# Kernel tuning notes

Measured on AMD Instinct MI355X. Metric: run time of the kernel, lower is better.

The kernel has to match this reference:

```python
import jax, jax.numpy as jnp
import numpy as np

N_EMB = 1024
N_HEAD = 16
HEAD_DIM = N_EMB // N_HEAD


def setup_inputs() -> dict:
    key = jax.random.key(0)
    ks = jax.random.split(key, 5)
    scale = 0.02
    x = jax.random.normal(ks[0], (2, 2048, N_EMB), dtype=jnp.float32)
    W_attn = jax.random.normal(ks[1], (N_EMB, 3 * N_EMB), dtype=jnp.float32) * scale
    b_attn = jnp.zeros((3 * N_EMB,), dtype=jnp.float32)
    W_proj = jax.random.normal(ks[2], (N_EMB, N_EMB), dtype=jnp.float32) * scale
    b_proj = jnp.zeros((N_EMB,), dtype=jnp.float32)
    return {"x": x, "W_attn": W_attn, "b_attn": b_attn, "W_proj": W_proj, "b_proj": b_proj}


def reference(x, W_attn, b_attn, W_proj, b_proj):
    B, T, C = x.shape
    qkv = x @ W_attn + b_attn  # [B, T, 3C]
    q, k, v = jnp.split(qkv, 3, axis=-1)
    # [B, H, T, Dh]
    q = q.reshape(B, T, N_HEAD, HEAD_DIM).transpose(0, 2, 1, 3)
    k = k.reshape(B, T, N_HEAD, HEAD_DIM).transpose(0, 2, 1, 3)
    v = v.reshape(B, T, N_HEAD, HEAD_DIM).transpose(0, 2, 1, 3)
    scale = 1.0 / jnp.sqrt(jnp.float32(HEAD_DIM))
    attn = jnp.einsum('bhqd,bhkd->bhqk', q, k) * scale  # [B, H, T, T]
    causal = jnp.tril(jnp.ones((T, T), dtype=bool))
    attn = jnp.where(causal[None, None], attn, -jnp.inf)
    attn = jax.nn.softmax(attn, axis=-1)
    y = jnp.einsum('bhqk,bhkd->bhqd', attn, v)  # [B, H, T, Dh]
    y = y.transpose(0, 2, 1, 3).reshape(B, T, C)
    return y @ W_proj + b_proj
```

## Files before the change

kernel.cpp:

```cpp
#include <hip/hip_runtime.h>
#include <hip/hip_bf16.h>

typedef __bf16 bf16;
typedef __attribute__((ext_vector_type(2))) __bf16 bf16x2;
typedef __attribute__((ext_vector_type(4))) __bf16 bf16x4;
typedef __attribute__((ext_vector_type(8))) __bf16 bf16x8;
typedef __attribute__((ext_vector_type(4))) float f32x4;
typedef __attribute__((ext_vector_type(16))) float f32x16;
typedef unsigned int u32;
typedef __attribute__((ext_vector_type(4))) u32 u32x4;
typedef const __attribute__((address_space(1))) u32* gptr_t;
typedef __attribute__((address_space(3))) u32* lptr_t;

#define N_EMB 1024
#define N_HEAD 16
#define HEAD_DIM 64
#define T_SEQ 2048
#define BATCH 2
#define M_TOT (BATCH * T_SEQ)
#define N_QKV (3 * N_EMB)
#define KDIM 1024
#define CS_LOG2E 0.1803368801111129f

__device__ inline unsigned short f2bu(float f) {
    unsigned u = __builtin_bit_cast(unsigned, f);
    return (unsigned short)((u + 0x7fffu + ((u >> 16) & 1u)) >> 16);
}
__device__ inline bf16 f2b(float f) {
    unsigned short s = f2bu(f);
    return __builtin_bit_cast(bf16, s);
}
__device__ inline u32 pkbf(float lo, float hi) {
    bf16x2 t; t[0] = (bf16)lo; t[1] = (bf16)hi;
    return __builtin_bit_cast(u32, t);
}
__device__ __forceinline__ float xhalf_max(float x) {
    return fmaxf(x, __shfl_xor(x, 32, 64));
}
__device__ __forceinline__ float xhalf_sum(float x) {
    return x + __shfl_xor(x, 32, 64);
}

__global__ __launch_bounds__(256) void k_cast(const float* __restrict__ x,
                                              bf16* __restrict__ xb, int n4) {
    int i = blockIdx.x * 256 + threadIdx.x;
    if (i < n4) {
        float4 v = reinterpret_cast<const float4*>(x)[i];
        ushort4 u;
        u.x = f2bu(v.x); u.y = f2bu(v.y); u.z = f2bu(v.z); u.w = f2bu(v.w);
        reinterpret_cast<ushort4*>(xb)[i] = u;
    }
}

__global__ __launch_bounds__(256) void k_transpose(const float* __restrict__ W,
                                                   bf16* __restrict__ Wt,
                                                   int K, int N) {
    __shared__ float tile[32][33];
    int k0 = blockIdx.x * 32;
    int n0 = blockIdx.y * 32;
    int tx = threadIdx.x & 31;
    int ty = threadIdx.x >> 5;
    for (int j = 0; j < 32; j += 8)
        tile[ty + j][tx] = W[(k0 + ty + j) * N + n0 + tx];
    __syncthreads();
    for (int j = 0; j < 32; j += 8)
        Wt[(n0 + ty + j) * (long)K + k0 + tx] = f2b(tile[tx][ty + j]);
}

__global__ __launch_bounds__(256) void k_vtrans(const bf16* __restrict__ v,
                                                bf16* __restrict__ vt) {
    __shared__ bf16 tile[64 * 76];
    const int bh = blockIdx.y;
    const int t0 = blockIdx.x * 64;
    const bf16* src = v + (size_t)bh * T_SEQ * HEAD_DIM;
    bf16* dst = vt + (size_t)bh * HEAD_DIM * T_SEQ;
    const int tid = threadIdx.x;
    #pragma unroll
    for (int it = 0; it < 2; ++it) {
        const int row = (tid >> 3) + it * 32;
        const int col = (tid & 7) * 8;
        bf16x8 val = *reinterpret_cast<const bf16x8*>(src + (size_t)(t0 + row) * HEAD_DIM + col);
        bf16x4 lo;  lo[0] = val[0]; lo[1] = val[1]; lo[2] = val[2]; lo[3] = val[3];
        bf16x4 hiv; hiv[0] = val[4]; hiv[1] = val[5]; hiv[2] = val[6]; hiv[3] = val[7];
        *reinterpret_cast<bf16x4*>(&tile[row * 76 + col]) = lo;
        *reinterpret_cast<bf16x4*>(&tile[row * 76 + col + 4]) = hiv;
    }
    __syncthreads();
    #pragma unroll
    for (int it = 0; it < 2; ++it) {
        const int d  = (tid >> 3) + it * 32;
        const int tt = (tid & 7) * 8;
        bf16x8 val;
        #pragma unroll
        for (int q = 0; q < 8; ++q)
            val[q] = tile[(tt + q) * 76 + d];
        *reinterpret_cast<bf16x8*>(dst + (size_t)d * T_SEQ + t0 + tt) = val;
    }
}

#define GEMM_MAINLOOP(A_, Bt_, m0_, n0_)                                          \
    __shared__ __align__(16) bf16 As[128 * 32];                                   \
    __shared__ __align__(16) bf16 Bs[128 * 32];                                   \
    const int lane = threadIdx.x & 63;                                            \
    const int w    = threadIdx.x >> 6;                                            \
    const int wr   = w >> 1;                                                      \
    const int wc   = w & 1;                                                       \
    const int r    = lane & 15;                                                   \
    const int ko   = (lane >> 4) * 8;                                             \
    const int srow = w * 32 + (lane >> 2);                                        \
    const int sk   = (lane & 3) * 8;                                              \
    const bf16* a_g0 = A_ + (size_t)(m0_ + srow) * KDIM + sk;                     \
    const bf16* a_g1 = a_g0 + 16 * KDIM;                                          \
    const bf16* b_g0 = Bt_ + (size_t)(n0_ + srow) * KDIM + sk;                    \
    const bf16* b_g1 = b_g0 + 16 * KDIM;                                          \
    bf16* a_l0 = As + (w * 2) * 512;                                              \
    bf16* a_l1 = As + (w * 2 + 1) * 512;                                          \
    bf16* b_l0 = Bs + (w * 2) * 512;                                              \
    bf16* b_l1 = Bs + (w * 2 + 1) * 512;                                          \
    f32x4 acc[4][4];                                                              \
    for (int i = 0; i < 4; ++i)                                                   \
        for (int j = 0; j < 4; ++j) acc[i][j] = (f32x4){0.f, 0.f, 0.f, 0.f};      \
    for (int k0 = 0; k0 < KDIM; k0 += 32) {                                       \
        __builtin_amdgcn_global_load_lds((gptr_t)(const void*)(a_g0 + k0),        \
                                         (lptr_t)(void*)a_l0, 16, 0, 0);          \
        __builtin_amdgcn_global_load_lds((gptr_t)(const void*)(a_g1 + k0),        \
                                         (lptr_t)(void*)a_l1, 16, 0, 0);          \
        __builtin_amdgcn_global_load_lds((gptr_t)(const void*)(b_g0 + k0),        \
                                         (lptr_t)(void*)b_l0, 16, 0, 0);          \
        __builtin_amdgcn_global_load_lds((gptr_t)(const void*)(b_g1 + k0),        \
                                         (lptr_t)(void*)b_l1, 16, 0, 0);          \
        __syncthreads();                                                          \
        bf16x8 af[4], bfr[4];                                                     \
        for (int m = 0; m < 4; ++m)                                               \
            af[m] = *reinterpret_cast<const bf16x8*>(As + (wr * 64 + m * 16 + r) * 32 + ko); \
        for (int n = 0; n < 4; ++n)                                               \
            bfr[n] = *reinterpret_cast<const bf16x8*>(Bs + (wc * 64 + n * 16 + r) * 32 + ko); \
        for (int m = 0; m < 4; ++m)                                               \
            for (int n = 0; n < 4; ++n)                                           \
                acc[m][n] = __builtin_amdgcn_mfma_f32_16x16x32_bf16(af[m], bfr[n], acc[m][n], 0, 0, 0); \
        __syncthreads();                                                          \
    }

#define GEMM_MAINLOOP_64(A_, Bt_, m0_, n0_)                                       \
    __shared__ __align__(16) bf16 As[64 * 32];                                    \
    __shared__ __align__(16) bf16 Bs[128 * 32];                                   \
    const int lane = threadIdx.x & 63;                                            \
    const int w    = threadIdx.x >> 6;                                            \
    const int wr   = w >> 1;                                                      \
    const int wc   = w & 1;                                                       \
    const int r    = lane & 15;                                                   \
    const int ko   = (lane >> 4) * 8;                                             \
    const int srow = w * 16 + (lane >> 2);                                        \
    const int sk   = (lane & 3) * 8;                                              \
    const bf16* a_g0 = A_ + (size_t)(m0_ + srow) * KDIM + sk;                     \
    const bf16* b_g0 = Bt_ + (size_t)(n0_ + srow) * KDIM + sk;                    \
    const bf16* b_g1 = b_g0 + 64 * KDIM;                                          \
    bf16* a_l0 = As + w * 512;                                                    \
    bf16* b_l0 = Bs + w * 512;                                                    \
    bf16* b_l1 = Bs + 64 * 32 + w * 512;                                          \
    f32x4 acc[2][4];                                                              \
    for (int i = 0; i < 2; ++i)                                                   \
        for (int j = 0; j < 4; ++j) acc[i][j] = (f32x4){0.f, 0.f, 0.f, 0.f};      \
    for (int k0 = 0; k0 < KDIM; k0 += 32) {                                       \
        __builtin_amdgcn_global_load_lds((gptr_t)(const void*)(a_g0 + k0),        \
                                         (lptr_t)(void*)a_l0, 16, 0, 0);          \
        __builtin_amdgcn_global_load_lds((gptr_t)(const void*)(b_g0 + k0),        \
                                         (lptr_t)(void*)b_l0, 16, 0, 0);          \
        __builtin_amdgcn_global_load_lds((gptr_t)(const void*)(b_g1 + k0),        \
                                         (lptr_t)(void*)b_l1, 16, 0, 0);          \
        __syncthreads();                                                          \
        bf16x8 af[2], bfr[4];                                                     \
        for (int m = 0; m < 2; ++m)                                               \
            af[m] = *reinterpret_cast<const bf16x8*>(As + (wr * 32 + m * 16 + r) * 32 + ko); \
        for (int n = 0; n < 4; ++n)                                               \
            bfr[n] = *reinterpret_cast<const bf16x8*>(Bs + (wc * 64 + n * 16 + r) * 32 + ko); \
        for (int m = 0; m < 2; ++m)                                               \
            for (int n = 0; n < 4; ++n)                                           \
                acc[m][n] = __builtin_amdgcn_mfma_f32_16x16x32_bf16(af[m], bfr[n], acc[m][n], 0, 0, 0); \
        __syncthreads();                                                          \
    }

__global__ __launch_bounds__(256) void k_gemm_qkv(const bf16* __restrict__ A,
                                                  const bf16* __restrict__ Bt,
                                                  const float* __restrict__ bias,
                                                  bf16* __restrict__ qb,
                                                  bf16* __restrict__ kb,
                                                  bf16* __restrict__ vb) {
    const int m0 = blockIdx.x * 128;
    const int n0 = blockIdx.y * 128;
    GEMM_MAINLOOP(A, Bt, m0, n0)
    const int col   = lane & 15;
    const int rbase = (lane >> 4) * 4;
    for (int nn = 0; nn < 4; ++nn) {
        int n = n0 + wc * 64 + nn * 16 + col;
        float bv = bias[n];
        int which = n >> 10;
        int c  = n & 1023;
        int h  = c >> 6;
        int dh = c & 63;
        bf16* dst = (which == 0) ? qb : ((which == 1) ? kb : vb);
        const float sc = (which == 0) ? CS_LOG2E : 1.0f;
        for (int mm = 0; mm < 4; ++mm) {
            for (int i = 0; i < 4; ++i) {
                int m = m0 + wr * 64 + mm * 16 + rbase + i;
                int b_ = m >> 11;
                int t  = m & 2047;
                dst[(((b_ * N_HEAD + h) * T_SEQ) + t) * HEAD_DIM + dh] =
                    f2b((acc[mm][nn][i] + bv) * sc);
            }
        }
    }
}

__global__ __launch_bounds__(256) void k_gemm_proj(const bf16* __restrict__ A,
                                                   const bf16* __restrict__ Bt,
                                                   const float* __restrict__ bias,
                                                   float* __restrict__ out) {
    const int m0 = blockIdx.x * 64;
    const int n0 = blockIdx.y * 128;
    GEMM_MAINLOOP_64(A, Bt, m0, n0)
    const int col   = lane & 15;
    const int rbase = (lane >> 4) * 4;
    for (int nn = 0; nn < 4; ++nn) {
        int n = n0 + wc * 64 + nn * 16 + col;
        float bv = bias[n];
        for (int mm = 0; mm < 2; ++mm) {
            for (int i = 0; i < 4; ++i) {
                int m = m0 + wr * 32 + mm * 16 + rbase + i;
                out[(size_t)m * N_EMB + n] = acc[mm][nn][i] + bv;
            }
        }
    }
}

__device__ __forceinline__ void pv_group(const float* p, int hi,
                                         const bf16x8 (&va)[2][2], f32x16 (&o)[2]) {
    u32 c[8], sw[8];
    #pragma unroll
    for (int i = 0; i < 8; ++i) c[i] = pkbf(p[2 * i], p[2 * i + 1]);
    #pragma unroll
    for (int i = 0; i < 8; ++i) sw[i] = __shfl_xor(c[i], 32, 64);
    u32x4 f0, f1;
    f0[0] = hi ? sw[2] : c[0];  f0[1] = hi ? sw[3] : c[1];
    f0[2] = hi ? c[2]  : sw[0]; f0[3] = hi ? c[3]  : sw[1];
    f1[0] = hi ? sw[6] : c[4];  f1[1] = hi ? sw[7] : c[5];
    f1[2] = hi ? c[6]  : sw[4]; f1[3] = hi ? c[7]  : sw[5];
    bf16x8 pb0 = __builtin_bit_cast(bf16x8, f0);
    bf16x8 pb1 = __builtin_bit_cast(bf16x8, f1);
    __builtin_amdgcn_s_setprio(1);
    #pragma unroll
    for (int dt = 0; dt < 2; ++dt) {
        o[dt] = __builtin_amdgcn_mfma_f32_32x32x16_bf16(va[dt][0], pb0, o[dt], 0, 0, 0);
        o[dt] = __builtin_amdgcn_mfma_f32_32x32x16_bf16(va[dt][1], pb1, o[dt], 0, 0, 0);
    }
    __builtin_amdgcn_s_setprio(0);
}

__device__ __forceinline__ void load_va(const bf16* __restrict__ Vt, int kbase,
                                        int qr, int hi, bf16x8 (&va)[2][2]) {
    #pragma unroll
    for (int dt = 0; dt < 2; ++dt)
        #pragma unroll
        for (int ks = 0; ks < 2; ++ks)
            va[dt][ks] = *reinterpret_cast<const bf16x8*>(
                Vt + (size_t)(dt * 32 + qr) * T_SEQ + kbase + ks * 16 + hi * 8);
}

__device__ __forceinline__ float tree_max16(const f32x16& v) {
    float a0 = fmaxf(v[0], v[1]),   a1 = fmaxf(v[2], v[3]);
    float a2 = fmaxf(v[4], v[5]),   a3 = fmaxf(v[6], v[7]);
    float a4 = fmaxf(v[8], v[9]),   a5 = fmaxf(v[10], v[11]);
    float a6 = fmaxf(v[12], v[13]), a7 = fmaxf(v[14], v[15]);
    float b0 = fmaxf(a0, a1), b1 = fmaxf(a2, a3);
    float b2 = fmaxf(a4, a5), b3 = fmaxf(a6, a7);
    return fmaxf(fmaxf(b0, b1), fmaxf(b2, b3));
}

template<bool DIAG_HI>
__device__ __forceinline__ void attn_tile64(
    const bf16* __restrict__ K, const bf16* __restrict__ Vt, int kbase,
    int qr, int hi, const bf16x8 (&qf)[4],
    float& m_r, float& l_r, f32x16 (&o)[2]) {
    bf16x8 kf0[4], kf1[4];
    #pragma unroll
    for (int f = 0; f < 4; ++f) {
        kf0[f] = *reinterpret_cast<const bf16x8*>(
            K + (size_t)(kbase + qr) * HEAD_DIM + f * 16 + hi * 8);
        kf1[f] = *reinterpret_cast<const bf16x8*>(
            K + (size_t)(kbase + 32 + qr) * HEAD_DIM + f * 16 + hi * 8);
    }
    f32x16 st0, st1;
    #pragma unroll
    for (int r = 0; r < 16; ++r) { st0[r] = 0.f; st1[r] = 0.f; }
    __builtin_amdgcn_s_setprio(1);
    #pragma unroll
    for (int f = 0; f < 4; ++f)
        st0 = __builtin_amdgcn_mfma_f32_32x32x16_bf16(kf0[f], qf[f], st0, 0, 0, 0);
    #pragma unroll
    for (int f = 0; f < 4; ++f)
        st1 = __builtin_amdgcn_mfma_f32_32x32x16_bf16(kf1[f], qf[f], st1, 0, 0, 0);
    __builtin_amdgcn_s_setprio(0);
    if (DIAG_HI) {
        const int kp4 = 4 * hi;
        #pragma unroll
        for (int r = 0; r < 16; ++r) {
            const int kpos = (r & 3) + 8 * (r >> 2) + kp4;
            if (kpos > qr) st1[r] = -3.0e38f;
        }
    }
    float mt = fmaxf(tree_max16(st0), tree_max16(st1));
    mt = xhalf_max(mt);
    if (!__all(mt <= m_r + 8.f)) {
        const float mn = fmaxf(m_r, mt);
        const float alpha = exp2f(m_r - mn);
        m_r = mn;
        l_r *= alpha;
        #pragma unroll
        for (int r = 0; r < 16; ++r) { o[0][r] *= alpha; o[1][r] *= alpha; }
    }
    bf16x8 va0[2][2];
    load_va(Vt, kbase, qr, hi, va0);
    float p0[16], p1[16];
    #pragma unroll
    for (int r = 0; r < 16; ++r) { p0[r] = exp2f(st0[r] - m_r); }
    #pragma unroll
    for (int r = 0; r < 16; ++r) { p1[r] = exp2f(st1[r] - m_r); }
    float s0 = 0.f, s1 = 0.f;
    #pragma unroll
    for (int r = 0; r < 8; ++r) { s0 += p0[r] + p0[r + 8]; s1 += p1[r] + p1[r + 8]; }
    l_r += xhalf_sum(s0 + s1);
    pv_group(p0, hi, va0, o);
    bf16x8 va1[2][2];
    load_va(Vt, kbase + 32, qr, hi, va1);
    pv_group(p1, hi, va1, o);
}

template<bool DIAG_MASK>
__device__ __forceinline__ void attn_tile32(
    const bf16* __restrict__ K, const bf16* __restrict__ Vt, int kbase,
    int qr, int hi, const bf16x8 (&qf)[4],
    float& m_r, float& l_r, f32x16 (&o)[2]) {
    bf16x8 kf[4];
    #pragma unroll
    for (int f = 0; f < 4; ++f)
        kf[f] = *reinterpret_cast<const bf16x8*>(
            K + (size_t)(kbase + qr) * HEAD_DIM + f * 16 + hi * 8);
    f32x16 st;
    #pragma unroll
    for (int r = 0; r < 16; ++r) st[r] = 0.f;
    __builtin_amdgcn_s_setprio(1);
    #pragma unroll
    for (int f = 0; f < 4; ++f)
        st = __builtin_amdgcn_mfma_f32_32x32x16_bf16(kf[f], qf[f], st, 0, 0, 0);
    __builtin_amdgcn_s_setprio(0);
    if (DIAG_MASK) {
        const int kp4 = 4 * hi;
        #pragma unroll
        for (int r = 0; r < 16; ++r) {
            const int kpos = (r & 3) + 8 * (r >> 2) + kp4;
            if (kpos > qr) st[r] = -3.0e38f;
        }
    }
    float mt = xhalf_max(tree_max16(st));
    if (!__all(mt <= m_r + 8.f)) {
        const float mn = fmaxf(m_r, mt);
        const float alpha = exp2f(m_r - mn);
        m_r = mn;
        l_r *= alpha;
        #pragma unroll
        for (int r = 0; r < 16; ++r) { o[0][r] *= alpha; o[1][r] *= alpha; }
    }
    bf16x8 va[2][2];
    load_va(Vt, kbase, qr, hi, va);
    float p[16];
    #pragma unroll
    for (int r = 0; r < 16; ++r) p[r] = exp2f(st[r] - m_r);
    float s = 0.f;
    #pragma unroll
    for (int r = 0; r < 8; ++r) s += p[r] + p[r + 8];
    l_r += xhalf_sum(s);
    pv_group(p, hi, va, o);
}

__global__ __launch_bounds__(128, 3) void k_attn(const bf16* __restrict__ qb,
                                                 const bf16* __restrict__ kb,
                                                 const bf16* __restrict__ vtb,
                                                 bf16* __restrict__ yb) {
    const int lane = threadIdx.x & 63;
    const int wv   = threadIdx.x >> 6;
    const int bh   = blockIdx.x;
    const int qblk = 63 - blockIdx.y;
    const int q0   = qblk * 32;
    const int b    = bh >> 4;
    const int h    = bh & 15;

    const bf16* Q  = qb  + (size_t)bh * T_SEQ * HEAD_DIM;
    const bf16* K  = kb  + (size_t)bh * T_SEQ * HEAD_DIM;
    const bf16* Vt = vtb + (size_t)bh * HEAD_DIM * T_SEQ;

    const int qr = lane & 31;
    const int hi = lane >> 5;

    bf16x8 qf[4];
    #pragma unroll
    for (int f = 0; f < 4; ++f)
        qf[f] = *reinterpret_cast<const bf16x8*>(
            Q + (size_t)(q0 + qr) * HEAD_DIM + f * 16 + hi * 8);

    f32x16 o[2];
    #pragma unroll
    for (int r = 0; r < 16; ++r) { o[0][r] = 0.f; o[1][r] = 0.f; }
    float m_r = -3.0e38f, l_r = 0.f;

    const int n  = qblk + 1;
    const int h0 = n - (n >> 1);
    const int lo  = wv ? h0 : 0;
    const int end = wv ? n  : h0;
    const bool has_diag = (end == n) && (end > lo);
    const int nd_end = has_diag ? end - 1 : end;

    int t = lo;
    while (t + 2 <= nd_end) {
        attn_tile64<false>(K, Vt, t * 32, qr, hi, qf, m_r, l_r, o);
        t += 2;
    }
    if (has_diag) {
        if (nd_end - t == 1)
            attn_tile64<true>(K, Vt, t * 32, qr, hi, qf, m_r, l_r, o);
        else
            attn_tile32<true>(K, Vt, qblk * 32, qr, hi, qf, m_r, l_r, o);
    } else if (t < end) {
        attn_tile32<false>(K, Vt, t * 32, qr, hi, qf, m_r, l_r, o);
    }

    __shared__ float ls_o[64][33];
    __shared__ float ls_m[64];
    __shared__ float ls_l[64];
    if (wv == 1) {
        #pragma unroll
        for (int i = 0; i < 16; ++i) {
            ls_o[lane][i]      = o[0][i];
            ls_o[lane][16 + i] = o[1][i];
        }
        ls_m[lane] = m_r;
        ls_l[lane] = l_r;
    }
    __syncthreads();
    if (wv == 1) return;
    const float m1 = ls_m[lane];
    const float l1 = ls_l[lane];
    const float mN = fmaxf(m_r, m1);
    const float a0 = exp2f(m_r - mN);
    const float a1 = (m1 > -1.0e37f) ? exp2f(m1 - mN) : 0.f;
    l_r = l_r * a0 + l1 * a1;
    #pragma unroll
    for (int i = 0; i < 16; ++i) {
        o[0][i] = o[0][i] * a0 + ls_o[lane][i]      * a1;
        o[1][i] = o[1][i] * a0 + ls_o[lane][16 + i] * a1;
    }

    const float inv = 1.f / fmaxf(l_r, 1e-30f);
    const int tq = q0 + qr;
    bf16* yrow = yb + ((size_t)(b * T_SEQ + tq)) * N_EMB + h * HEAD_DIM;
    #pragma unroll
    for (int dt = 0; dt < 2; ++dt) {
        #pragma unroll
        for (int rr = 0; rr < 4; ++rr) {
            const int d0 = dt * 32 + 8 * rr + 4 * hi;
            ushort4 u;
            u.x = f2bu(o[dt][4 * rr + 0] * inv);
            u.y = f2bu(o[dt][4 * rr + 1] * inv);
            u.z = f2bu(o[dt][4 * rr + 2] * inv);
            u.w = f2bu(o[dt][4 * rr + 3] * inv);
            *reinterpret_cast<ushort4*>(yrow + d0) = u;
        }
    }
}

extern "C" void kernel_launch(void* const* d_in, const int* in_sizes, int n_in,
                              void* d_out, int out_size, void* d_ws, size_t ws_size,
                              hipStream_t stream) {
    const float* x      = (const float*)d_in[0];
    const float* W_attn = (const float*)d_in[1];
    const float* b_attn = (const float*)d_in[2];
    const float* W_proj = (const float*)d_in[3];
    const float* b_proj = (const float*)d_in[4];
    float* out = (float*)d_out;

    const size_t sz_x   = (size_t)M_TOT * N_EMB;
    const size_t sz_wat = (size_t)N_QKV * N_EMB;
    const size_t sz_wpt = (size_t)N_EMB * N_EMB;
    const size_t sz_hd  = (size_t)BATCH * N_HEAD * T_SEQ * HEAD_DIM;
    const size_t need = (sz_x + sz_wat + sz_wpt + 3 * sz_hd + sz_x) * sizeof(bf16);
    if (ws_size < need) return;

    bf16* xb  = (bf16*)d_ws;
    bf16* wat = xb + sz_x;
    bf16* wpt = wat + sz_wat;
    bf16* qb  = wpt + sz_wpt;
    bf16* kbf = qb + sz_hd;
    bf16* vbf = kbf + sz_hd;
    bf16* yb  = vbf + sz_hd;
    bf16* vtb = xb;

    k_cast<<<dim3((sz_x / 4 + 255) / 256), 256, 0, stream>>>(x, xb, (int)(sz_x / 4));
    k_transpose<<<dim3(N_EMB / 32, N_QKV / 32), 256, 0, stream>>>(W_attn, wat, N_EMB, N_QKV);
    k_transpose<<<dim3(N_EMB / 32, N_EMB / 32), 256, 0, stream>>>(W_proj, wpt, N_EMB, N_EMB);
    k_gemm_qkv<<<dim3(M_TOT / 128, N_QKV / 128), 256, 0, stream>>>(xb, wat, b_attn, qb, kbf, vbf);
    k_vtrans<<<dim3(T_SEQ / 64, BATCH * N_HEAD), 256, 0, stream>>>(vbf, vtb);
    k_attn<<<dim3(BATCH * N_HEAD, 64), 128, 0, stream>>>(qb, kbf, vtb, yb);
    k_gemm_proj<<<dim3(M_TOT / 64, N_EMB / 128), 256, 0, stream>>>(yb, wpt, b_proj, out);
}
```

Baseline: 139.2 us.

## Split attention KV range across four waves per query block instead of two

```diff
diff --git a/kernel.cpp b/kernel.cpp
--- a/kernel.cpp
+++ b/kernel.cpp
@@ -382,10 +382,10 @@
     pv_group(p, hi, va, o);
 }
 
-__global__ __launch_bounds__(128, 3) void k_attn(const bf16* __restrict__ qb,
-                                                 const bf16* __restrict__ kb,
-                                                 const bf16* __restrict__ vtb,
-                                                 bf16* __restrict__ yb) {
+__global__ __launch_bounds__(256) void k_attn(const bf16* __restrict__ qb,
+                                              const bf16* __restrict__ kb,
+                                              const bf16* __restrict__ vtb,
+                                              bf16* __restrict__ yb) {
     const int lane = threadIdx.x & 63;
     const int wv   = threadIdx.x >> 6;
     const int bh   = blockIdx.x;
@@ -412,11 +412,13 @@
     for (int r = 0; r < 16; ++r) { o[0][r] = 0.f; o[1][r] = 0.f; }
     float m_r = -3.0e38f, l_r = 0.f;
 
-    const int n  = qblk + 1;
-    const int h0 = n - (n >> 1);
-    const int lo  = wv ? h0 : 0;
-    const int end = wv ? n  : h0;
-    const bool has_diag = (end == n) && (end > lo);
+    const int n    = qblk + 1;
+    const int base = n >> 2;
+    const int rem  = n & 3;
+    const int lo   = wv * base + (wv < rem ? wv : rem);
+    const int cnt  = base + (wv < rem ? 1 : 0);
+    const int end  = lo + cnt;
+    const bool has_diag = (end == n) && (cnt > 0);
     const int nd_end = has_diag ? end - 1 : end;
 
     int t = lo;
@@ -428,35 +430,41 @@
         if (nd_end - t == 1)
             attn_tile64<true>(K, Vt, t * 32, qr, hi, qf, m_r, l_r, o);
         else
-            attn_tile32<true>(K, Vt, qblk * 32, qr, hi, qf, m_r, l_r, o);
+            attn_tile32<true>(K, Vt, (n - 1) * 32, qr, hi, qf, m_r, l_r, o);
     } else if (t < end) {
         attn_tile32<false>(K, Vt, t * 32, qr, hi, qf, m_r, l_r, o);
     }
 
-    __shared__ float ls_o[64][33];
-    __shared__ float ls_m[64];
-    __shared__ float ls_l[64];
-    if (wv == 1) {
+    __shared__ float ls_o[3][64][33];
+    __shared__ float ls_m[3][64];
+    __shared__ float ls_l[3][64];
+    if (wv > 0) {
         #pragma unroll
         for (int i = 0; i < 16; ++i) {
-            ls_o[lane][i]      = o[0][i];
-            ls_o[lane][16 + i] = o[1][i];
-        }
-        ls_m[lane] = m_r;
-        ls_l[lane] = l_r;
+            ls_o[wv - 1][lane][i]      = o[0][i];
+            ls_o[wv - 1][lane][16 + i] = o[1][i];
+        }
+        ls_m[wv - 1][lane] = m_r;
+        ls_l[wv - 1][lane] = l_r;
     }
     __syncthreads();
-    if (wv == 1) return;
-    const float m1 = ls_m[lane];
-    const float l1 = ls_l[lane];
-    const float mN = fmaxf(m_r, m1);
-    const float a0 = exp2f(m_r - mN);
-    const float a1 = (m1 > -1.0e37f) ? exp2f(m1 - mN) : 0.f;
-    l_r = l_r * a0 + l1 * a1;
-    #pragma unroll
-    for (int i = 0; i < 16; ++i) {
-        o[0][i] = o[0][i] * a0 + ls_o[lane][i]      * a1;
-        o[1][i] = o[1][i] * a0 + ls_o[lane][16 + i] * a1;
+    if (wv > 0) return;
+    #pragma unroll
+    for (int s = 0; s < 3; ++s) {
+        const float m1 = ls_m[s][lane];
+        if (m1 > -1.0e37f) {
+            const float l1 = ls_l[s][lane];
+            const float mN = fmaxf(m_r, m1);
+            const float a0 = exp2f(m_r - mN);
+            const float a1 = exp2f(m1 - mN);
+            l_r = l_r * a0 + l1 * a1;
+            #pragma unroll
+            for (int i = 0; i < 16; ++i) {
+                o[0][i] = o[0][i] * a0 + ls_o[s][lane][i]      * a1;
+                o[1][i] = o[1][i] * a0 + ls_o[s][lane][16 + i] * a1;
+            }
+            m_r = mN;
+        }
     }
 
     const float inv = 1.f / fmaxf(l_r, 1e-30f);
@@ -508,6 +516,6 @@
     k_transpose<<<dim3(N_EMB / 32, N_EMB / 32), 256, 0, stream>>>(W_proj, wpt, N_EMB, N_EMB);
     k_gemm_qkv<<<dim3(M_TOT / 128, N_QKV / 128), 256, 0, stream>>>(xb, wat, b_attn, qb, kbf, vbf);
     k_vtrans<<<dim3(T_SEQ / 64, BATCH * N_HEAD), 256, 0, stream>>>(vbf, vtb);
-    k_attn<<<dim3(BATCH * N_HEAD, 64), 128, 0, stream>>>(qb, kbf, vtb, yb);
+    k_attn<<<dim3(BATCH * N_HEAD, 64), 256, 0, stream>>>(qb, kbf, vtb, yb);
     k_gemm_proj<<<dim3(M_TOT / 64, N_EMB / 128), 256, 0, stream>>>(yb, wpt, b_proj, out);
 }
```

Result: no change. 140.9 us (+1.2%).
